# Kernel optimization log

Measured on AMD Instinct MI355X. Metric: run time of the kernel, lower is better.

Reference implementation:

```python
import jax, jax.numpy as jnp
import numpy as np

IN_F = 1024
OUT_F = 1024
N_ORDER = 13  # grid_size=10 + spline_order=3
RMS_EPS = 1e-6


def setup_inputs() -> dict:
    key = jax.random.key(0)
    k_x, k_b, k_p = jax.random.split(key, 3)
    x = jax.random.normal(k_x, (4, 2048, IN_F), dtype=jnp.float32)
    # flax param init: normal(stddev=scale_base/sqrt(in_features)) etc.
    base_weight = jax.random.normal(k_b, (IN_F, OUT_F), dtype=jnp.float32) * (1.0 / np.sqrt(IN_F))
    poly_weight = jax.random.normal(k_p, (N_ORDER, IN_F, OUT_F), dtype=jnp.float32) * (0.1 / np.sqrt(IN_F * N_ORDER))
    rms_scale = jnp.ones((OUT_F,), dtype=jnp.float32)  # nn.RMSNorm default scale init
    return {"x": x, "base_weight": base_weight, "poly_weight": poly_weight, "rms_scale": rms_scale}


def reference(x, base_weight, poly_weight, rms_scale):
    orig_dtype = x.dtype
    prefix = x.shape[:-1]
    x_2d = x.reshape(-1, IN_F)  # [B, in]

    # Base path: SiLU(x) @ W_base in bf16
    x_c = x_2d.astype(jnp.bfloat16)
    out = jax.nn.silu(x_c) @ base_weight.astype(jnp.bfloat16)  # [B, out] bf16

    # Chebyshev recursion on tanh-normalized fp32 input
    x_safe = jnp.tanh(x_2d.astype(jnp.float32))
    pw = poly_weight.astype(jnp.bfloat16)
    T_prev = jnp.ones_like(x_safe)
    T_curr = x_safe
    out = out + T_prev.astype(jnp.bfloat16) @ pw[0]
    out = out + T_curr.astype(jnp.bfloat16) @ pw[1]
    for k in range(2, N_ORDER):  # fixed small unroll (13 orders)
        T_next = 2.0 * x_safe * T_curr - T_prev
        out = out + T_next.astype(jnp.bfloat16) @ pw[k]
        T_prev = T_curr
        T_curr = T_next

    # RMSNorm (flax default: eps=1e-6, learned scale)
    o32 = out.astype(jnp.float32)
    ms = jnp.mean(o32 * o32, axis=-1, keepdims=True)
    o32 = o32 * jax.lax.rsqrt(ms + RMS_EPS) * rms_scale
    return o32.astype(orig_dtype).reshape(prefix + (OUT_F,))
```

## Files before the change

### kernel.cpp

```cpp
#include <hip/hip_runtime.h>
#include <cstdint>

#define IN_F  1024
#define OUT_F 1024
#define NORD  13
#define BROWS 8192

typedef __bf16 bf16x8 __attribute__((ext_vector_type(8)));
typedef float  f32x4  __attribute__((ext_vector_type(4)));
typedef unsigned short u16x8 __attribute__((ext_vector_type(8)));
typedef unsigned short u16x4 __attribute__((ext_vector_type(4)));

__device__ __forceinline__ unsigned short f2bf(float f) {
  unsigned int u = __float_as_uint(f);
  unsigned int r = u + 0x7FFFu + ((u >> 16) & 1u);
  return (unsigned short)(r >> 16);
}
__device__ __forceinline__ float bf2f(unsigned short h) {
  return __uint_as_float(((unsigned int)h) << 16);
}
__device__ __forceinline__ float bfround(float f) { return bf2f(f2bf(f)); }

__device__ __forceinline__ void gload_lds16(const void* g, void* l) {
  __builtin_amdgcn_global_load_lds(
      (__attribute__((address_space(1))) unsigned int*)(uintptr_t)g,
      (__attribute__((address_space(3))) unsigned int*)(unsigned int)(uintptr_t)l,
      16, 0, 0);
}

__global__ __launch_bounds__(256)
void act_kernel(const float* __restrict__ x, unsigned short* __restrict__ A,
                int b0, int nb, int Kp) {
  int t   = threadIdx.x;
  int row = blockIdx.x * 2 + (t >> 7);
  int f0  = (t & 127) * 8;
  const float* xr = x + (size_t)row * IN_F + f0;
  float xv[8];
  *(float4*)&xv[0] = *(const float4*)&xr[0];
  *(float4*)&xv[4] = *(const float4*)&xr[4];
  unsigned short* Ar = A + (size_t)row * Kp;
  int omax = b0 + nb - 1;
  if (b0 == 0) {
    u16x8 sv;
#pragma unroll
    for (int i = 0; i < 8; i++) {
      float xc = bfround(xv[i]);
      float sg = bfround(1.0f / (1.0f + expf(-xc)));
      sv[i] = f2bf(xc * sg);
    }
    *(u16x8*)&Ar[f0] = sv;
  }
  float xs[8], tp[8], tc[8];
#pragma unroll
  for (int i = 0; i < 8; i++) { xs[i] = tanhf(xv[i]); tp[i] = 1.0f; tc[i] = xs[i]; }
  for (int o = 1; o <= omax; o++) {
    if (o >= b0) {
      int bb = o - b0;
      u16x8 sv;
#pragma unroll
      for (int i = 0; i < 8; i++) sv[i] = f2bf(tc[i]);
      *(u16x8*)&Ar[(size_t)bb * 1024 + f0] = sv;
    }
    {
#pragma clang fp contract(off)
#pragma unroll
      for (int i = 0; i < 8; i++) {
        float tm = 2.0f * xs[i] * tc[i];
        float tn = tm - tp[i];
        tp[i] = tc[i]; tc[i] = tn;
      }
    }
  }
}

__global__ __launch_bounds__(256)
void wprep_kernel(const float* __restrict__ baseW, const float* __restrict__ poly,
                  unsigned short* __restrict__ Wt, int b0, int Kp) {
  __shared__ float tile[64][65];
  int bb = blockIdx.z;
  int g  = b0 + bb;
  const float* src = (g == 0) ? baseW : (poly + (size_t)g * (IN_F * OUT_F));
  int n0 = blockIdx.x * 64, f0 = blockIdx.y * 64;
  int tx = threadIdx.x, ty = threadIdx.y;
#pragma unroll
  for (int i = 0; i < 16; i++)
    tile[ty + i * 4][tx] = src[(size_t)(f0 + ty + i * 4) * OUT_F + n0 + tx];
  __syncthreads();
#pragma unroll
  for (int i = 0; i < 16; i++)
    Wt[(size_t)(n0 + ty + i * 4) * Kp + (size_t)bb * 1024 + f0 + tx] = f2bf(tile[tx][ty + i * 4]);
}

__global__ __launch_bounds__(256)
void bias1_kernel(const float* __restrict__ pw0, float* __restrict__ partial) {
  int t  = threadIdx.x;
  int n  = blockIdx.x * 256 + t;
  int fc = blockIdx.y;
  float s = 0.f;
  for (int f = fc * 128; f < fc * 128 + 128; f++)
    s += bf2f(f2bf(pw0[(size_t)f * OUT_F + n]));
  partial[(size_t)fc * OUT_F + n] = s;
}
__global__ __launch_bounds__(256)
void bias2_kernel(const float* __restrict__ partial, float* __restrict__ bias) {
  int n = blockIdx.x * 256 + threadIdx.x;
  float s = 0.f;
#pragma unroll
  for (int fc = 0; fc < 8; fc++) s += partial[(size_t)fc * OUT_F + n];
  bias[n] = s;
}

__global__ __launch_bounds__(256, 2)
void gemm_kernel(const unsigned short* __restrict__ A, const unsigned short* __restrict__ Wt,
                 unsigned short* __restrict__ outAcc, const float* __restrict__ bias,
                 int Kp, int isFirst) {
  __shared__ unsigned short sA[2][128 * 64];
  __shared__ unsigned short sB[2][128 * 64];
  int t    = threadIdx.x;
  int m0   = blockIdx.x * 128;
  int n0   = blockIdx.y * 128;
  int wave = t >> 6, lane = t & 63;
  int lr   = lane & 15, quad = lane >> 4;
  int wm   = (wave & 1) * 64, wn = (wave >> 1) * 64;

  int rs = t >> 3;
  int jg = (t & 7) ^ (rs & 7);
  const unsigned short* aSrc = A  + (size_t)(m0 + rs) * Kp + jg * 8;
  const unsigned short* bSrc = Wt + (size_t)(n0 + rs) * Kp + jg * 8;
  char* sAc = (char*)sA;
  char* sBc = (char*)sB;
  int ldsOff = t * 16;

  int aOff[4][2], bOff[4][2];
#pragma unroll
  for (int mi = 0; mi < 4; mi++) {
    int row = wm + mi * 16 + lr;
#pragma unroll
    for (int ks = 0; ks < 2; ks++) {
      int j = ks * 4 + quad;
      aOff[mi][ks] = row * 128 + ((j ^ (row & 7)) * 16);
    }
  }
#pragma unroll
  for (int ni = 0; ni < 4; ni++) {
    int row = wn + ni * 16 + lr;
#pragma unroll
    for (int ks = 0; ks < 2; ks++) {
      int j = ks * 4 + quad;
      bOff[ni][ks] = row * 128 + ((j ^ (row & 7)) * 16);
    }
  }

  f32x4 s[4][4];
  float bsr[4];
  if (isFirst) {
#pragma unroll
    for (int ni = 0; ni < 4; ni++) bsr[ni] = bfround(bias[n0 + wn + ni * 16 + lr]);
  } else {
#pragma unroll
    for (int ni = 0; ni < 4; ni++) {
      int gn = n0 + wn + ni * 16 + lr;
#pragma unroll
      for (int mi = 0; mi < 4; mi++) {
        int gmBase = m0 + wm + mi * 16 + quad * 4;
#pragma unroll
        for (int r = 0; r < 4; r++)
          s[mi][ni][r] = bf2f(outAcc[(size_t)(gmBase + r) * OUT_F + gn]);
      }
    }
  }

  int nKt  = Kp >> 6;
  int nBlk = Kp >> 10;

  auto stage = [&](int gkt, int buf) {
    const unsigned short* aP = aSrc + gkt * 64;
    const unsigned short* bP = bSrc + gkt * 64;
    char* dA = sAc + buf * 16384 + ldsOff;
    char* dB = sBc + buf * 16384 + ldsOff;
#pragma unroll
    for (int rd = 0; rd < 4; rd++)
      gload_lds16(aP + (size_t)rd * 32 * Kp, dA + rd * 4096);
#pragma unroll
    for (int rd = 0; rd < 4; rd++)
      gload_lds16(bP + (size_t)rd * 32 * Kp, dB + rd * 4096);
  };

  stage(0, 0);

  int gkt = 0;
  for (int blk = 0; blk < nBlk; blk++) {
    f32x4 acc[4][4];
#pragma unroll
    for (int mi = 0; mi < 4; mi++)
#pragma unroll
      for (int ni = 0; ni < 4; ni++)
        acc[mi][ni] = (f32x4){0.f, 0.f, 0.f, 0.f};

    for (int kt = 0; kt < 16; kt++, gkt++) {
      __syncthreads();
      int nxt = gkt + 1;
      if (nxt < nKt) stage(nxt, nxt & 1);
      int buf = gkt & 1;
      char* bA = sAc + buf * 16384;
      char* bB = sBc + buf * 16384;
#pragma unroll
      for (int ks = 0; ks < 2; ks++) {
        bf16x8 af[4], bfr[4];
#pragma unroll
        for (int mi = 0; mi < 4; mi++) af[mi] = *(const bf16x8*)(bA + aOff[mi][ks]);
#pragma unroll
        for (int ni = 0; ni < 4; ni++) bfr[ni] = *(const bf16x8*)(bB + bOff[ni][ks]);
#pragma unroll
        for (int mi = 0; mi < 4; mi++)
#pragma unroll
          for (int ni = 0; ni < 4; ni++)
            acc[mi][ni] = __builtin_amdgcn_mfma_f32_16x16x32_bf16(af[mi], bfr[ni], acc[mi][ni], 0, 0, 0);
      }
    }

    bool firstBlk = (isFirst && blk == 0);
    if (firstBlk) {
#pragma unroll
      for (int mi = 0; mi < 4; mi++)
#pragma unroll
        for (int ni = 0; ni < 4; ni++)
#pragma unroll
          for (int r = 0; r < 4; r++) {
            float p = bfround(acc[mi][ni][r]);
            s[mi][ni][r] = bfround(p + bsr[ni]);
          }
    } else {
#pragma unroll
      for (int mi = 0; mi < 4; mi++)
#pragma unroll
        for (int ni = 0; ni < 4; ni++)
#pragma unroll
          for (int r = 0; r < 4; r++)
            s[mi][ni][r] = bfround(s[mi][ni][r] + bfround(acc[mi][ni][r]));
    }
  }

#pragma unroll
  for (int ni = 0; ni < 4; ni++) {
    int gn = n0 + wn + ni * 16 + lr;
#pragma unroll
    for (int mi = 0; mi < 4; mi++) {
      int gmBase = m0 + wm + mi * 16 + quad * 4;
#pragma unroll
      for (int r = 0; r < 4; r++)
        outAcc[(size_t)(gmBase + r) * OUT_F + gn] = f2bf(s[mi][ni][r]);
    }
  }
}

__global__ __launch_bounds__(256)
void rms_kernel(const unsigned short* __restrict__ outAcc, const float* __restrict__ scale,
                float* __restrict__ out) {
  int row = blockIdx.x;
  int t   = threadIdx.x;
  const unsigned short* src = outAcc + (size_t)row * OUT_F;
  u16x4 hv = *(const u16x4*)&src[t * 4];
  float v[4];
#pragma unroll
  for (int i = 0; i < 4; i++) v[i] = bf2f(hv[i]);
  float s = v[0]*v[0] + v[1]*v[1] + v[2]*v[2] + v[3]*v[3];
#pragma unroll
  for (int off = 32; off > 0; off >>= 1) s += __shfl_down(s, off, 64);
  __shared__ float red[4];
  if ((t & 63) == 0) red[t >> 6] = s;
  __syncthreads();
  float tot = red[0] + red[1] + red[2] + red[3];
  float sc = 1.0f / sqrtf(tot * (1.0f / OUT_F) + 1e-6f);
  float4 so = *(const float4*)&scale[t * 4];
  float4 o;
  o.x = v[0] * sc * so.x; o.y = v[1] * sc * so.y;
  o.z = v[2] * sc * so.z; o.w = v[3] * sc * so.w;
  *(float4*)&out[(size_t)row * OUT_F + t * 4] = o;
}

extern "C" void kernel_launch(void* const* d_in, const int* in_sizes, int n_in,
                              void* d_out, int out_size, void* d_ws, size_t ws_size,
                              hipStream_t stream) {
  const float* x     = (const float*)d_in[0];
  const float* baseW = (const float*)d_in[1];
  const float* poly  = (const float*)d_in[2];
  const float* scale = (const float*)d_in[3];
  float* out = (float*)d_out;

  char* ws = (char*)d_ws;
  unsigned short* outAcc = (unsigned short*)ws;
  float* bias    = (float*)(ws + 16777216);
  float* partial = (float*)(ws + 16777216 + 4096);
  size_t fixed   = 16777216 + 4096 + 32768;

  int CHB = 1;
  for (int c = NORD; c >= 1; c--) {
    size_t need = fixed + (size_t)c * 1024 * OUT_F * 2
                + (size_t)BROWS * c * 1024 * 2;
    if (need <= ws_size) { CHB = c; break; }
  }
  unsigned short* Wt = (unsigned short*)(ws + fixed);
  unsigned short* Ap = (unsigned short*)(ws + fixed + (size_t)CHB * 1024 * OUT_F * 2);

  bias1_kernel<<<dim3(4, 8), 256, 0, stream>>>(poly, partial);
  bias2_kernel<<<4, 256, 0, stream>>>(partial, bias);

  for (int b0 = 0; b0 < NORD; b0 += CHB) {
    int nb = (CHB < NORD - b0) ? CHB : (NORD - b0);
    int Kp = nb * 1024;
    act_kernel<<<BROWS / 2, 256, 0, stream>>>(x, Ap, b0, nb, Kp);
    wprep_kernel<<<dim3(16, 16, nb), dim3(64, 4), 0, stream>>>(baseW, poly, Wt, b0, Kp);
    gemm_kernel<<<dim3(BROWS / 128, 8), 256, 0, stream>>>(Ap, Wt, outAcc, bias, Kp, (b0 == 0) ? 1 : 0);
  }
  rms_kernel<<<BROWS, 256, 0, stream>>>(outAcc, scale, out);
}
```

Baseline: 405.5 us.

## Fuse activation, weight prep and bias reduction into one prep kernel

Merges the activation-expansion kernel, the weight transpose/convert kernel and the first bias-partial kernel into a single launch that dispatches on block index. The second bias reduction moves into the GEMM prologue, which now sums the 8 partials itself. The weight transpose also switches to float4 loads and 16-byte packed bf16 stores. This removes several kernel launches and their serialization gaps, and lets the independent prep work overlap, at the cost of a more branchy kernel whose block types have different resource needs.

```diff
diff --git a/kernel.cpp b/kernel.cpp
--- a/kernel.cpp
+++ b/kernel.cpp
@@ -29,90 +29,98 @@
 }
 
 __global__ __launch_bounds__(256)
-void act_kernel(const float* __restrict__ x, unsigned short* __restrict__ A,
-                int b0, int nb, int Kp) {
+void prep_kernel(const float* __restrict__ x, const float* __restrict__ baseW,
+                 const float* __restrict__ poly, unsigned short* __restrict__ A,
+                 unsigned short* __restrict__ Wt, float* __restrict__ partial,
+                 int b0, int nb, int Kp) {
+  int bid = blockIdx.x;
   int t   = threadIdx.x;
-  int row = blockIdx.x * 2 + (t >> 7);
-  int f0  = (t & 127) * 8;
-  const float* xr = x + (size_t)row * IN_F + f0;
-  float xv[8];
-  *(float4*)&xv[0] = *(const float4*)&xr[0];
-  *(float4*)&xv[4] = *(const float4*)&xr[4];
-  unsigned short* Ar = A + (size_t)row * Kp;
-  int omax = b0 + nb - 1;
-  if (b0 == 0) {
-    u16x8 sv;
-#pragma unroll
-    for (int i = 0; i < 8; i++) {
-      float xc = bfround(xv[i]);
-      float sg = bfround(1.0f / (1.0f + expf(-xc)));
-      sv[i] = f2bf(xc * sg);
-    }
-    *(u16x8*)&Ar[f0] = sv;
-  }
-  float xs[8], tp[8], tc[8];
-#pragma unroll
-  for (int i = 0; i < 8; i++) { xs[i] = tanhf(xv[i]); tp[i] = 1.0f; tc[i] = xs[i]; }
-  for (int o = 1; o <= omax; o++) {
-    if (o >= b0) {
-      int bb = o - b0;
+
+  if (bid < 4096) {
+    int row = bid * 2 + (t >> 7);
+    int f0  = (t & 127) * 8;
+    const float* xr = x + (size_t)row * IN_F + f0;
+    float xv[8];
+    *(float4*)&xv[0] = *(const float4*)&xr[0];
+    *(float4*)&xv[4] = *(const float4*)&xr[4];
+    unsigned short* Ar = A + (size_t)row * Kp;
+    int omax = b0 + nb - 1;
+    if (b0 == 0) {
       u16x8 sv;
 #pragma unroll
-      for (int i = 0; i < 8; i++) sv[i] = f2bf(tc[i]);
-      *(u16x8*)&Ar[(size_t)bb * 1024 + f0] = sv;
-    }
-    {
+      for (int i = 0; i < 8; i++) {
+        float xc = bfround(xv[i]);
+        float sg = bfround(1.0f / (1.0f + expf(-xc)));
+        sv[i] = f2bf(xc * sg);
+      }
+      *(u16x8*)&Ar[f0] = sv;
+    }
+    float xs[8], tp[8], tc[8];
+#pragma unroll
+    for (int i = 0; i < 8; i++) { xs[i] = tanhf(xv[i]); tp[i] = 1.0f; tc[i] = xs[i]; }
+    for (int o = 1; o <= omax; o++) {
+      if (o >= b0) {
+        int bb = o - b0;
+        u16x8 sv;
+#pragma unroll
+        for (int i = 0; i < 8; i++) sv[i] = f2bf(tc[i]);
+        *(u16x8*)&Ar[(size_t)bb * 1024 + f0] = sv;
+      }
+      {
 #pragma clang fp contract(off)
 #pragma unroll
-      for (int i = 0; i < 8; i++) {
-        float tm = 2.0f * xs[i] * tc[i];
-        float tn = tm - tp[i];
-        tp[i] = tc[i]; tc[i] = tn;
-      }
-    }
-  }
-}
-
-__global__ __launch_bounds__(256)
-void wprep_kernel(const float* __restrict__ baseW, const float* __restrict__ poly,
-                  unsigned short* __restrict__ Wt, int b0, int Kp) {
-  __shared__ float tile[64][65];
-  int bb = blockIdx.z;
-  int g  = b0 + bb;
-  const float* src = (g == 0) ? baseW : (poly + (size_t)g * (IN_F * OUT_F));
-  int n0 = blockIdx.x * 64, f0 = blockIdx.y * 64;
-  int tx = threadIdx.x, ty = threadIdx.y;
-#pragma unroll
-  for (int i = 0; i < 16; i++)
-    tile[ty + i * 4][tx] = src[(size_t)(f0 + ty + i * 4) * OUT_F + n0 + tx];
-  __syncthreads();
-#pragma unroll
-  for (int i = 0; i < 16; i++)
-    Wt[(size_t)(n0 + ty + i * 4) * Kp + (size_t)bb * 1024 + f0 + tx] = f2bf(tile[tx][ty + i * 4]);
-}
-
-__global__ __launch_bounds__(256)
-void bias1_kernel(const float* __restrict__ pw0, float* __restrict__ partial) {
-  int t  = threadIdx.x;
-  int n  = blockIdx.x * 256 + t;
-  int fc = blockIdx.y;
+        for (int i = 0; i < 8; i++) {
+          float tm = 2.0f * xs[i] * tc[i];
+          float tn = tm - tp[i];
+          tp[i] = tc[i]; tc[i] = tn;
+        }
+      }
+    }
+    return;
+  }
+
+  if (bid < 4096 + 256 * nb) {
+    __shared__ float tile[64][65];
+    int w   = bid - 4096;
+    int bb  = w >> 8;
+    int rem = w & 255;
+    int n0  = (rem & 15) * 64;
+    int f0  = (rem >> 4) * 64;
+    int g   = b0 + bb;
+    const float* src = (g == 0) ? baseW : (poly + (size_t)g * (IN_F * OUT_F));
+    int fl = t >> 4, n4 = (t & 15) * 4;
+#pragma unroll
+    for (int i = 0; i < 4; i++) {
+      int f = fl + 16 * i;
+      float4 v = *(const float4*)&src[(size_t)(f0 + f) * OUT_F + n0 + n4];
+      tile[f][n4 + 0] = v.x; tile[f][n4 + 1] = v.y;
+      tile[f][n4 + 2] = v.z; tile[f][n4 + 3] = v.w;
+    }
+    __syncthreads();
+    int f8 = (t & 7) * 8, nl = t >> 3;
+#pragma unroll
+    for (int i = 0; i < 2; i++) {
+      int n = nl + 32 * i;
+      u16x8 o;
+#pragma unroll
+      for (int j = 0; j < 8; j++) o[j] = f2bf(tile[f8 + j][n]);
+      *(u16x8*)&Wt[(size_t)(n0 + n) * Kp + (size_t)bb * 1024 + f0 + f8] = o;
+    }
+    return;
+  }
+
+  int w2 = bid - (4096 + 256 * nb);
+  int n  = (w2 & 3) * 256 + t;
+  int fc = w2 >> 2;
   float s = 0.f;
   for (int f = fc * 128; f < fc * 128 + 128; f++)
-    s += bf2f(f2bf(pw0[(size_t)f * OUT_F + n]));
+    s += bf2f(f2bf(poly[(size_t)f * OUT_F + n]));
   partial[(size_t)fc * OUT_F + n] = s;
-}
-__global__ __launch_bounds__(256)
-void bias2_kernel(const float* __restrict__ partial, float* __restrict__ bias) {
-  int n = blockIdx.x * 256 + threadIdx.x;
-  float s = 0.f;
-#pragma unroll
-  for (int fc = 0; fc < 8; fc++) s += partial[(size_t)fc * OUT_F + n];
-  bias[n] = s;
 }
 
 __global__ __launch_bounds__(256, 2)
 void gemm_kernel(const unsigned short* __restrict__ A, const unsigned short* __restrict__ Wt,
-                 unsigned short* __restrict__ outAcc, const float* __restrict__ bias,
+                 unsigned short* __restrict__ outAcc, const float* __restrict__ partial,
                  int Kp, int isFirst) {
   __shared__ unsigned short sA[2][128 * 64];
   __shared__ unsigned short sB[2][128 * 64];
@@ -155,7 +163,13 @@
   float bsr[4];
   if (isFirst) {
 #pragma unroll
-    for (int ni = 0; ni < 4; ni++) bsr[ni] = bfround(bias[n0 + wn + ni * 16 + lr]);
+    for (int ni = 0; ni < 4; ni++) {
+      int gn = n0 + wn + ni * 16 + lr;
+      float bsum = 0.f;
+#pragma unroll
+      for (int fc = 0; fc < 8; fc++) bsum += partial[(size_t)fc * OUT_F + gn];
+      bsr[ni] = bfround(bsum);
+    }
   } else {
 #pragma unroll
     for (int ni = 0; ni < 4; ni++) {
@@ -290,9 +304,8 @@
 
   char* ws = (char*)d_ws;
   unsigned short* outAcc = (unsigned short*)ws;
-  float* bias    = (float*)(ws + 16777216);
-  float* partial = (float*)(ws + 16777216 + 4096);
-  size_t fixed   = 16777216 + 4096 + 32768;
+  float* partial = (float*)(ws + 16777216);
+  size_t fixed   = 16777216 + 32768;
 
   int CHB = 1;
   for (int c = NORD; c >= 1; c--) {
@@ -303,15 +316,12 @@
   unsigned short* Wt = (unsigned short*)(ws + fixed);
   unsigned short* Ap = (unsigned short*)(ws + fixed + (size_t)CHB * 1024 * OUT_F * 2);
 
-  bias1_kernel<<<dim3(4, 8), 256, 0, stream>>>(poly, partial);
-  bias2_kernel<<<4, 256, 0, stream>>>(partial, bias);
-
   for (int b0 = 0; b0 < NORD; b0 += CHB) {
     int nb = (CHB < NORD - b0) ? CHB : (NORD - b0);
     int Kp = nb * 1024;
-    act_kernel<<<BROWS / 2, 256, 0, stream>>>(x, Ap, b0, nb, Kp);
-    wprep_kernel<<<dim3(16, 16, nb), dim3(64, 4), 0, stream>>>(baseW, poly, Wt, b0, Kp);
-    gemm_kernel<<<dim3(BROWS / 128, 8), 256, 0, stream>>>(Ap, Wt, outAcc, bias, Kp, (b0 == 0) ? 1 : 0);
+    int nBias = (b0 == 0) ? 32 : 0;
+    prep_kernel<<<4096 + 256 * nb + nBias, 256, 0, stream>>>(x, baseW, poly, Ap, Wt, partial, b0, nb, Kp);
+    gemm_kernel<<<dim3(BROWS / 128, 8), 256, 0, stream>>>(Ap, Wt, outAcc, partial, Kp, (b0 == 0) ? 1 : 0);
   }
   rms_kernel<<<BROWS, 256, 0, stream>>>(outAcc, scale, out);
 }
```

Result: slower. 437.8 us (+8.0%).

## Load GEMM A fragments directly to registers and vectorize weight transpose

Applied to the files above, without the earlier changes.

The GEMM no longer stages the activation tile through LDS. Each wave loads its A fragments straight from global memory into registers, double-buffered across k-steps, while B is still staged through LDS. This halves LDS traffic and footprint, which could help occupancy, but it drops A reuse across the two waves that share rows, so global/L2 load traffic rises and latency is exposed. The weight-prep transpose also switches to float4 reads and 16-byte bf16 writes to improve coalescing.

```diff
diff --git a/kernel.cpp b/kernel.cpp
--- a/kernel.cpp
+++ b/kernel.cpp
@@ -81,14 +81,25 @@
   int g  = b0 + bb;
   const float* src = (g == 0) ? baseW : (poly + (size_t)g * (IN_F * OUT_F));
   int n0 = blockIdx.x * 64, f0 = blockIdx.y * 64;
-  int tx = threadIdx.x, ty = threadIdx.y;
-#pragma unroll
-  for (int i = 0; i < 16; i++)
-    tile[ty + i * 4][tx] = src[(size_t)(f0 + ty + i * 4) * OUT_F + n0 + tx];
+  int t  = threadIdx.x;
+  int fl = t >> 4, n4 = (t & 15) * 4;
+#pragma unroll
+  for (int i = 0; i < 4; i++) {
+    int f = fl + 16 * i;
+    float4 v = *(const float4*)&src[(size_t)(f0 + f) * OUT_F + n0 + n4];
+    tile[f][n4 + 0] = v.x; tile[f][n4 + 1] = v.y;
+    tile[f][n4 + 2] = v.z; tile[f][n4 + 3] = v.w;
+  }
   __syncthreads();
-#pragma unroll
-  for (int i = 0; i < 16; i++)
-    Wt[(size_t)(n0 + ty + i * 4) * Kp + (size_t)bb * 1024 + f0 + tx] = f2bf(tile[tx][ty + i * 4]);
+  int f8 = (t & 7) * 8, nl = t >> 3;
+#pragma unroll
+  for (int i = 0; i < 2; i++) {
+    int n = nl + 32 * i;
+    u16x8 o;
+#pragma unroll
+    for (int j = 0; j < 8; j++) o[j] = f2bf(tile[f8 + j][n]);
+    *(u16x8*)&Wt[(size_t)(n0 + n) * Kp + (size_t)bb * 1024 + f0 + f8] = o;
+  }
 }
 
 __global__ __launch_bounds__(256)
@@ -114,7 +125,6 @@
 void gemm_kernel(const unsigned short* __restrict__ A, const unsigned short* __restrict__ Wt,
                  unsigned short* __restrict__ outAcc, const float* __restrict__ bias,
                  int Kp, int isFirst) {
-  __shared__ unsigned short sA[2][128 * 64];
   __shared__ unsigned short sB[2][128 * 64];
   int t    = threadIdx.x;
   int m0   = blockIdx.x * 128;
@@ -125,22 +135,16 @@
 
   int rs = t >> 3;
   int jg = (t & 7) ^ (rs & 7);
-  const unsigned short* aSrc = A  + (size_t)(m0 + rs) * Kp + jg * 8;
   const unsigned short* bSrc = Wt + (size_t)(n0 + rs) * Kp + jg * 8;
-  char* sAc = (char*)sA;
   char* sBc = (char*)sB;
   int ldsOff = t * 16;
 
-  int aOff[4][2], bOff[4][2];
-#pragma unroll
-  for (int mi = 0; mi < 4; mi++) {
-    int row = wm + mi * 16 + lr;
-#pragma unroll
-    for (int ks = 0; ks < 2; ks++) {
-      int j = ks * 4 + quad;
-      aOff[mi][ks] = row * 128 + ((j ^ (row & 7)) * 16);
-    }
-  }
+  size_t aRow[4];
+#pragma unroll
+  for (int mi = 0; mi < 4; mi++)
+    aRow[mi] = (size_t)(m0 + wm + mi * 16 + lr) * Kp + quad * 8;
+
+  int bOff[4][2];
 #pragma unroll
   for (int ni = 0; ni < 4; ni++) {
     int row = wn + ni * 16 + lr;
@@ -173,20 +177,25 @@
   int nKt  = Kp >> 6;
   int nBlk = Kp >> 10;
 
-  auto stage = [&](int gkt, int buf) {
-    const unsigned short* aP = aSrc + gkt * 64;
+  auto stageB = [&](int gkt, int buf) {
     const unsigned short* bP = bSrc + gkt * 64;
-    char* dA = sAc + buf * 16384 + ldsOff;
     char* dB = sBc + buf * 16384 + ldsOff;
-#pragma unroll
-    for (int rd = 0; rd < 4; rd++)
-      gload_lds16(aP + (size_t)rd * 32 * Kp, dA + rd * 4096);
 #pragma unroll
     for (int rd = 0; rd < 4; rd++)
       gload_lds16(bP + (size_t)rd * 32 * Kp, dB + rd * 4096);
   };
 
-  stage(0, 0);
+  bf16x8 aEv[4][2], aOd[4][2];
+  auto loadA = [&](int gkt, bf16x8 (&dst)[4][2]) {
+#pragma unroll
+    for (int mi = 0; mi < 4; mi++)
+#pragma unroll
+      for (int ks = 0; ks < 2; ks++)
+        dst[mi][ks] = *(const bf16x8*)(A + aRow[mi] + gkt * 64 + ks * 32);
+  };
+
+  stageB(0, 0);
+  loadA(0, aEv);
 
   int gkt = 0;
   for (int blk = 0; blk < nBlk; blk++) {
@@ -197,26 +206,29 @@
       for (int ni = 0; ni < 4; ni++)
         acc[mi][ni] = (f32x4){0.f, 0.f, 0.f, 0.f};
 
-    for (int kt = 0; kt < 16; kt++, gkt++) {
+    auto step = [&](bf16x8 (&cur)[4][2], bf16x8 (&nxt)[4][2]) {
       __syncthreads();
-      int nxt = gkt + 1;
-      if (nxt < nKt) stage(nxt, nxt & 1);
       int buf = gkt & 1;
-      char* bA = sAc + buf * 16384;
+      int nn  = gkt + 1;
+      if (nn < nKt) { stageB(nn, buf ^ 1); loadA(nn, nxt); }
       char* bB = sBc + buf * 16384;
 #pragma unroll
       for (int ks = 0; ks < 2; ks++) {
-        bf16x8 af[4], bfr[4];
-#pragma unroll
-        for (int mi = 0; mi < 4; mi++) af[mi] = *(const bf16x8*)(bA + aOff[mi][ks]);
+        bf16x8 bfr[4];
 #pragma unroll
         for (int ni = 0; ni < 4; ni++) bfr[ni] = *(const bf16x8*)(bB + bOff[ni][ks]);
 #pragma unroll
         for (int mi = 0; mi < 4; mi++)
 #pragma unroll
           for (int ni = 0; ni < 4; ni++)
-            acc[mi][ni] = __builtin_amdgcn_mfma_f32_16x16x32_bf16(af[mi], bfr[ni], acc[mi][ni], 0, 0, 0);
+            acc[mi][ni] = __builtin_amdgcn_mfma_f32_16x16x32_bf16(cur[mi][ks], bfr[ni], acc[mi][ni], 0, 0, 0);
       }
+      gkt++;
+    };
+
+    for (int kt2 = 0; kt2 < 8; kt2++) {
+      step(aEv, aOd);
+      step(aOd, aEv);
     }
 
     bool firstBlk = (isFirst && blk == 0);
@@ -310,7 +322,7 @@
     int nb = (CHB < NORD - b0) ? CHB : (NORD - b0);
     int Kp = nb * 1024;
     act_kernel<<<BROWS / 2, 256, 0, stream>>>(x, Ap, b0, nb, Kp);
-    wprep_kernel<<<dim3(16, 16, nb), dim3(64, 4), 0, stream>>>(baseW, poly, Wt, b0, Kp);
+    wprep_kernel<<<dim3(16, 16, nb), 256, 0, stream>>>(baseW, poly, Wt, b0, Kp);
     gemm_kernel<<<dim3(BROWS / 128, 8), 256, 0, stream>>>(Ap, Wt, outAcc, bias, Kp, (b0 == 0) ? 1 : 0);
   }
   rms_kernel<<<BROWS, 256, 0, stream>>>(outAcc, scale, out);
```

Result: slower. 637.6 us (+57.2%).
